# Optimization experiments

Measured on AMD Instinct MI355X. Metric: run time of the kernel, lower is better.

Reference implementation:

```python
import jax, jax.numpy as jnp
import numpy as np

B, T, D = 32, 512, 1024
EPS = 1e-12  # torch F.normalize eps


def smooth_l1(x):
    # nn.SmoothL1Loss default beta=1.0
    a = jnp.abs(x)
    return jnp.where(a < 1.0, 0.5 * x * x, a - 0.5)


def setup_inputs() -> dict:
    key = jax.random.key(0)
    k1, k2, k3, k4 = jax.random.split(key, 4)
    return {
        "word_targets": jax.random.normal(k1, (B, T, D), dtype=jnp.float32),
        "image_targets": jax.random.normal(k2, (B, D), dtype=jnp.float32),
        "preds": jax.random.normal(k3, (B, T, D), dtype=jnp.float32),
        "decode_lengths": jax.random.randint(k4, (B,), 1, T + 1, dtype=jnp.int32),
    }


def reference(word_targets, image_targets, preds, decode_lengths):
    # mask over valid (ragged) positions: [B, T]
    mask = (jnp.arange(T)[None, :] < decode_lengths[:, None]).astype(preds.dtype)
    lens = decode_lengths.astype(preds.dtype)  # [B]

    # word loss: per-sample mean of smooth_l1 over valid tokens x D
    sl1 = smooth_l1(preds - word_targets) * mask[:, :, None]  # [B,T,D]
    word_per_b = sl1.sum(axis=(1, 2)) / (lens * D)             # [B]
    word_loss = word_per_b.mean()

    # per-sentence means over valid tokens: [B, D]
    pred_mean = (preds * mask[:, :, None]).sum(axis=1) / lens[:, None]
    targ_mean = (word_targets * mask[:, :, None]).sum(axis=1) / lens[:, None]
    sentence_loss = smooth_l1(pred_mean - targ_mean).mean(axis=1).mean()

    # image embedding loss: compare pred sentence mean to L2-normalized image embedding
    norm = jnp.maximum(jnp.linalg.norm(image_targets, axis=-1, keepdims=True), EPS)
    img_norm = image_targets / norm
    image_loss = smooth_l1(pred_mean - img_norm).mean(axis=1).mean()

    return word_loss + sentence_loss + image_loss
```

## Files before the change

kernel.cpp:

```cpp
#include <hip/hip_runtime.h>
#include <math.h>

static constexpr int B_ = 32;
static constexpr int T_ = 512;
static constexpr int D_ = 1024;
static constexpr int NCH_ = 4;
static constexpr int TCH_ = T_ / NCH_;
static constexpr int NDQ_ = 4;
static constexpr float EPS_ = 1e-12f;

__device__ __forceinline__ float sl1f(float x) {
    float a = fabsf(x);
    return a < 1.0f ? 0.5f * x * x : a - 0.5f;
}

__device__ __forceinline__ float blockReduce256(float v, float* lds) {
#pragma unroll
    for (int o = 32; o > 0; o >>= 1) v += __shfl_down(v, o, 64);
    int wid = threadIdx.x >> 6, lane = threadIdx.x & 63;
    if (lane == 0) lds[wid] = v;
    __syncthreads();
    float tot = lds[0] + lds[1] + lds[2] + lds[3];
    __syncthreads();
    return tot;
}

__global__ __launch_bounds__(256, 2) void pass1_kernel(
    const float* __restrict__ preds, const float* __restrict__ wtarg,
    const int* __restrict__ lens,
    float* __restrict__ wsPred, float* __restrict__ wsTarg,
    float* __restrict__ wsSl1, float* __restrict__ out)
{
    __shared__ float4 redP[4][64];
    __shared__ float4 redT[4][64];
    __shared__ float lred[4];

    const int c = blockIdx.x, b = blockIdx.y, q = blockIdx.z;
    const int tid = threadIdx.x;
    if (c == 0 && b == 0 && q == 0 && tid == 0) out[0] = 0.f;

    const int len = lens[b];
    const int t0 = c * TCH_;
    if (t0 >= len) return;
    const int nrows = min(TCH_, len - t0);

    const int j = tid & 63;
    const int r4 = tid >> 6;

    const float4* pp = reinterpret_cast<const float4*>(preds)
                       + (size_t)(b * T_ + t0) * (D_ / 4) + q * 64 + j;
    const float4* pw = reinterpret_cast<const float4*>(wtarg)
                       + (size_t)(b * T_ + t0) * (D_ / 4) + q * 64 + j;

    float4 ps = make_float4(0.f, 0.f, 0.f, 0.f);
    float4 ts = make_float4(0.f, 0.f, 0.f, 0.f);
    float s = 0.f;

    if (nrows == TCH_) {
#pragma unroll
        for (int tt = 0; tt < 4; ++tt) {
            float4 p[8], w[8];
#pragma unroll
            for (int jj = 0; jj < 8; ++jj)
                p[jj] = pp[(size_t)(r4 + 4 * (tt * 8 + jj)) * (D_ / 4)];
#pragma unroll
            for (int jj = 0; jj < 8; ++jj)
                w[jj] = pw[(size_t)(r4 + 4 * (tt * 8 + jj)) * (D_ / 4)];
#pragma unroll
            for (int jj = 0; jj < 8; ++jj) {
                ps.x += p[jj].x; ps.y += p[jj].y; ps.z += p[jj].z; ps.w += p[jj].w;
                ts.x += w[jj].x; ts.y += w[jj].y; ts.z += w[jj].z; ts.w += w[jj].w;
                s += sl1f(p[jj].x - w[jj].x) + sl1f(p[jj].y - w[jj].y)
                   + sl1f(p[jj].z - w[jj].z) + sl1f(p[jj].w - w[jj].w);
            }
        }
    } else {
        for (int r = r4; r < nrows; r += 4) {
            float4 p = pp[(size_t)r * (D_ / 4)];
            float4 w = pw[(size_t)r * (D_ / 4)];
            ps.x += p.x; ps.y += p.y; ps.z += p.z; ps.w += p.w;
            ts.x += w.x; ts.y += w.y; ts.z += w.z; ts.w += w.w;
            s += sl1f(p.x - w.x) + sl1f(p.y - w.y) + sl1f(p.z - w.z) + sl1f(p.w - w.w);
        }
    }

    redP[r4][j] = ps;
    redT[r4][j] = ts;
    float tot = blockReduce256(s, lred);
    if (tid < 64) {
        float4 a0 = redP[0][tid], a1 = redP[1][tid], a2 = redP[2][tid], a3 = redP[3][tid];
        float4 ap = make_float4(a0.x + a1.x + a2.x + a3.x, a0.y + a1.y + a2.y + a3.y,
                                a0.z + a1.z + a2.z + a3.z, a0.w + a1.w + a2.w + a3.w);
        float4 b0 = redT[0][tid], b1 = redT[1][tid], b2 = redT[2][tid], b3 = redT[3][tid];
        float4 at = make_float4(b0.x + b1.x + b2.x + b3.x, b0.y + b1.y + b2.y + b3.y,
                                b0.z + b1.z + b2.z + b3.z, b0.w + b1.w + b2.w + b3.w);
        const size_t off = ((size_t)(b * NCH_ + c)) * (D_ / 4) + q * 64 + tid;
        reinterpret_cast<float4*>(wsPred)[off] = ap;
        reinterpret_cast<float4*>(wsTarg)[off] = at;
    }
    if (tid == 0) wsSl1[(b * NCH_ + c) * NDQ_ + q] = tot;
}

__global__ __launch_bounds__(256) void pass2_kernel(
    const float* __restrict__ img, const int* __restrict__ lens,
    const float* __restrict__ wsPred, const float* __restrict__ wsTarg,
    const float* __restrict__ wsSl1, float* __restrict__ out)
{
    __shared__ float lred[4];
    const int b = blockIdx.x, tid = threadIdx.x;
    const int len = lens[b];
    const float flen = (float)len;
    const int nc = (len + TCH_ - 1) / TCH_;

    const float4* img4 = reinterpret_cast<const float4*>(img);
    float4 im = img4[(size_t)b * (D_ / 4) + tid];
    float ss = im.x * im.x + im.y * im.y + im.z * im.z + im.w * im.w;
    float sumsq = blockReduce256(ss, lred);
    float inv_norm = 1.0f / fmaxf(sqrtf(sumsq), EPS_);

    float4 ps = make_float4(0.f, 0.f, 0.f, 0.f);
    float4 ts = make_float4(0.f, 0.f, 0.f, 0.f);
#pragma unroll
    for (int c = 0; c < NCH_; ++c) {
        if (c < nc) {
            const size_t off = ((size_t)(b * NCH_ + c)) * (D_ / 4) + tid;
            float4 p = reinterpret_cast<const float4*>(wsPred)[off];
            float4 w = reinterpret_cast<const float4*>(wsTarg)[off];
            ps.x += p.x; ps.y += p.y; ps.z += p.z; ps.w += p.w;
            ts.x += w.x; ts.y += w.y; ts.z += w.z; ts.w += w.w;
        }
    }

    const float pmx = ps.x / flen, pmy = ps.y / flen, pmz = ps.z / flen, pmw = ps.w / flen;
    const float tmx = ts.x / flen, tmy = ts.y / flen, tmz = ts.z / flen, tmw = ts.w / flen;

    float s = sl1f(pmx - tmx) + sl1f(pmy - tmy) + sl1f(pmz - tmz) + sl1f(pmw - tmw)
            + sl1f(pmx - im.x * inv_norm) + sl1f(pmy - im.y * inv_norm)
            + sl1f(pmz - im.z * inv_norm) + sl1f(pmw - im.w * inv_norm);
    float tot = blockReduce256(s, lred);

    float wv = 0.f;
    if (tid < NCH_ * NDQ_) {
        int c = tid >> 2;
        if (c < nc) wv = wsSl1[(b * NCH_ + c) * NDQ_ + (tid & 3)];
    }
    if (tid < 64) {
#pragma unroll
        for (int o = 32; o > 0; o >>= 1) wv += __shfl_down(wv, o, 64);
    }

    if (tid == 0) {
        float per_b = tot / (float)D_ + wv / (flen * (float)D_);
        atomicAdd(out, per_b * (1.0f / (float)B_));
    }
}

extern "C" void kernel_launch(void* const* d_in, const int* in_sizes, int n_in,
                              void* d_out, int out_size, void* d_ws, size_t ws_size,
                              hipStream_t stream) {
    const float* wtarg = (const float*)d_in[0];
    const float* img   = (const float*)d_in[1];
    const float* preds = (const float*)d_in[2];
    const int*   lens  = (const int*)d_in[3];
    float* out = (float*)d_out;

    float* wsPred = (float*)d_ws;
    float* wsTarg = wsPred + (size_t)B_ * NCH_ * D_;
    float* wsSl1  = wsTarg + (size_t)B_ * NCH_ * D_;

    pass1_kernel<<<dim3(NCH_, B_, NDQ_), 256, 0, stream>>>(
        preds, wtarg, lens, wsPred, wsTarg, wsSl1, out);
    pass2_kernel<<<B_, 256, 0, stream>>>(img, lens, wsPred, wsTarg, wsSl1, out);
}
```

Baseline: 28.66 us.

## Compact ragged work units with prefix scan and persistent grid-stride pass1

Replaces the fixed 4x32x4 grid, where blocks beyond a sample's length exit immediately, with a prefix-sum over per-sample valid windows that builds a compact list of work units (64-row window by 128-column slice). A fixed grid of 1024 blocks walks that list with binary search, so only valid rows are launched and the load is spread more evenly across CUs. Pass2 recomputes the same scan to gather the variable number of partials per sample. Smaller units raise occupancy but add per-unit scan, search and reduction overhead, plus more partial sums in the workspace.

```diff
diff --git a/kernel.cpp b/kernel.cpp
--- a/kernel.cpp
+++ b/kernel.cpp
@@ -4,9 +4,10 @@
 static constexpr int B_ = 32;
 static constexpr int T_ = 512;
 static constexpr int D_ = 1024;
-static constexpr int NCH_ = 4;
-static constexpr int TCH_ = T_ / NCH_;
-static constexpr int NDQ_ = 4;
+static constexpr int WROWS_ = 64;
+static constexpr int SLICE4_ = 32;
+static constexpr int NSL_ = (D_ / 4) / SLICE4_;
+static constexpr int GRID1_ = 1024;
 static constexpr float EPS_ = 1e-12f;
 
 __device__ __forceinline__ float sl1f(float x) {
@@ -25,80 +26,112 @@
     return tot;
 }
 
-__global__ __launch_bounds__(256, 2) void pass1_kernel(
+__global__ __launch_bounds__(256, 4) void pass1_kernel(
     const float* __restrict__ preds, const float* __restrict__ wtarg,
     const int* __restrict__ lens,
     float* __restrict__ wsPred, float* __restrict__ wsTarg,
     float* __restrict__ wsSl1, float* __restrict__ out)
 {
-    __shared__ float4 redP[4][64];
-    __shared__ float4 redT[4][64];
+    __shared__ float4 redP[8][SLICE4_];
+    __shared__ float4 redT[8][SLICE4_];
     __shared__ float lred[4];
-
-    const int c = blockIdx.x, b = blockIdx.y, q = blockIdx.z;
+    __shared__ int sEx[B_ + 1];
+    __shared__ int sNwin[B_];
+    __shared__ int sLen[B_];
+
     const int tid = threadIdx.x;
-    if (c == 0 && b == 0 && q == 0 && tid == 0) out[0] = 0.f;
-
-    const int len = lens[b];
-    const int t0 = c * TCH_;
-    if (t0 >= len) return;
-    const int nrows = min(TCH_, len - t0);
-
-    const int j = tid & 63;
-    const int r4 = tid >> 6;
-
-    const float4* pp = reinterpret_cast<const float4*>(preds)
-                       + (size_t)(b * T_ + t0) * (D_ / 4) + q * 64 + j;
-    const float4* pw = reinterpret_cast<const float4*>(wtarg)
-                       + (size_t)(b * T_ + t0) * (D_ / 4) + q * 64 + j;
-
-    float4 ps = make_float4(0.f, 0.f, 0.f, 0.f);
-    float4 ts = make_float4(0.f, 0.f, 0.f, 0.f);
-    float s = 0.f;
-
-    if (nrows == TCH_) {
-#pragma unroll
-        for (int tt = 0; tt < 4; ++tt) {
-            float4 p[8], w[8];
-#pragma unroll
-            for (int jj = 0; jj < 8; ++jj)
-                p[jj] = pp[(size_t)(r4 + 4 * (tt * 8 + jj)) * (D_ / 4)];
-#pragma unroll
-            for (int jj = 0; jj < 8; ++jj)
-                w[jj] = pw[(size_t)(r4 + 4 * (tt * 8 + jj)) * (D_ / 4)];
-#pragma unroll
-            for (int jj = 0; jj < 8; ++jj) {
-                ps.x += p[jj].x; ps.y += p[jj].y; ps.z += p[jj].z; ps.w += p[jj].w;
-                ts.x += w[jj].x; ts.y += w[jj].y; ts.z += w[jj].z; ts.w += w[jj].w;
-                s += sl1f(p[jj].x - w[jj].x) + sl1f(p[jj].y - w[jj].y)
-                   + sl1f(p[jj].z - w[jj].z) + sl1f(p[jj].w - w[jj].w);
+    if (blockIdx.x == 0 && tid == 0) out[0] = 0.f;
+
+    if (tid < 64) {
+        int len_t = (tid < B_) ? lens[tid] : 0;
+        int nwin = (len_t + WROWS_ - 1) / WROWS_;
+        int nu = nwin * NSL_;
+        int incl = nu;
+#pragma unroll
+        for (int o = 1; o < 64; o <<= 1) {
+            int u = __shfl_up(incl, o, 64);
+            if (tid >= o) incl += u;
+        }
+        if (tid < B_) { sEx[tid] = incl - nu; sNwin[tid] = nwin; sLen[tid] = len_t; }
+        if (tid == B_ - 1) sEx[B_] = incl;
+    }
+    __syncthreads();
+    const int total = sEx[B_];
+
+    const int j = tid & (SLICE4_ - 1);
+    const int r8 = tid >> 5;
+
+    for (int fu = blockIdx.x; fu < total; fu += GRID1_) {
+        int lo = 0, hi = B_;
+        while (hi - lo > 1) {
+            int mid = (lo + hi) >> 1;
+            if (sEx[mid] <= fu) lo = mid; else hi = mid;
+        }
+        const int b = lo;
+        const int rem = fu - sEx[b];
+        const int nwin = sNwin[b];
+        const int s = rem / nwin;
+        const int w = rem - s * nwin;
+        const int len = sLen[b];
+        const int t0 = w * WROWS_;
+        const int nr = min(WROWS_, len - t0);
+
+        const float4* pp = reinterpret_cast<const float4*>(preds)
+                           + (size_t)(b * T_ + t0) * (D_ / 4) + s * SLICE4_ + j;
+        const float4* pw = reinterpret_cast<const float4*>(wtarg)
+                           + (size_t)(b * T_ + t0) * (D_ / 4) + s * SLICE4_ + j;
+
+        float4 ps = make_float4(0.f, 0.f, 0.f, 0.f);
+        float4 ts = make_float4(0.f, 0.f, 0.f, 0.f);
+        float sl = 0.f;
+
+        if (nr == WROWS_) {
+            float4 p[8], wv[8];
+#pragma unroll
+            for (int k = 0; k < 8; ++k) p[k] = pp[(size_t)(r8 + 8 * k) * (D_ / 4)];
+#pragma unroll
+            for (int k = 0; k < 8; ++k) wv[k] = pw[(size_t)(r8 + 8 * k) * (D_ / 4)];
+#pragma unroll
+            for (int k = 0; k < 8; ++k) {
+                ps.x += p[k].x; ps.y += p[k].y; ps.z += p[k].z; ps.w += p[k].w;
+                ts.x += wv[k].x; ts.y += wv[k].y; ts.z += wv[k].z; ts.w += wv[k].w;
+                sl += sl1f(p[k].x - wv[k].x) + sl1f(p[k].y - wv[k].y)
+                    + sl1f(p[k].z - wv[k].z) + sl1f(p[k].w - wv[k].w);
             }
-        }
-    } else {
-        for (int r = r4; r < nrows; r += 4) {
-            float4 p = pp[(size_t)r * (D_ / 4)];
-            float4 w = pw[(size_t)r * (D_ / 4)];
-            ps.x += p.x; ps.y += p.y; ps.z += p.z; ps.w += p.w;
-            ts.x += w.x; ts.y += w.y; ts.z += w.z; ts.w += w.w;
-            s += sl1f(p.x - w.x) + sl1f(p.y - w.y) + sl1f(p.z - w.z) + sl1f(p.w - w.w);
-        }
-    }
-
-    redP[r4][j] = ps;
-    redT[r4][j] = ts;
-    float tot = blockReduce256(s, lred);
-    if (tid < 64) {
-        float4 a0 = redP[0][tid], a1 = redP[1][tid], a2 = redP[2][tid], a3 = redP[3][tid];
-        float4 ap = make_float4(a0.x + a1.x + a2.x + a3.x, a0.y + a1.y + a2.y + a3.y,
-                                a0.z + a1.z + a2.z + a3.z, a0.w + a1.w + a2.w + a3.w);
-        float4 b0 = redT[0][tid], b1 = redT[1][tid], b2 = redT[2][tid], b3 = redT[3][tid];
-        float4 at = make_float4(b0.x + b1.x + b2.x + b3.x, b0.y + b1.y + b2.y + b3.y,
-                                b0.z + b1.z + b2.z + b3.z, b0.w + b1.w + b2.w + b3.w);
-        const size_t off = ((size_t)(b * NCH_ + c)) * (D_ / 4) + q * 64 + tid;
-        reinterpret_cast<float4*>(wsPred)[off] = ap;
-        reinterpret_cast<float4*>(wsTarg)[off] = at;
-    }
-    if (tid == 0) wsSl1[(b * NCH_ + c) * NDQ_ + q] = tot;
+        } else {
+            for (int k = 0; k < 8; ++k) {
+                int r = r8 + 8 * k;
+                if (r < nr) {
+                    float4 p = pp[(size_t)r * (D_ / 4)];
+                    float4 wv = pw[(size_t)r * (D_ / 4)];
+                    ps.x += p.x; ps.y += p.y; ps.z += p.z; ps.w += p.w;
+                    ts.x += wv.x; ts.y += wv.y; ts.z += wv.z; ts.w += wv.w;
+                    sl += sl1f(p.x - wv.x) + sl1f(p.y - wv.y)
+                        + sl1f(p.z - wv.z) + sl1f(p.w - wv.w);
+                }
+            }
+        }
+
+        redP[r8][j] = ps;
+        redT[r8][j] = ts;
+        float tot = blockReduce256(sl, lred);
+
+        if (tid < SLICE4_) {
+            float4 ap = make_float4(0.f, 0.f, 0.f, 0.f);
+            float4 at = make_float4(0.f, 0.f, 0.f, 0.f);
+#pragma unroll
+            for (int k = 0; k < 8; ++k) {
+                float4 a = redP[k][tid], bb = redT[k][tid];
+                ap.x += a.x; ap.y += a.y; ap.z += a.z; ap.w += a.w;
+                at.x += bb.x; at.y += bb.y; at.z += bb.z; at.w += bb.w;
+            }
+            const size_t off = (size_t)fu * SLICE4_ + tid;
+            reinterpret_cast<float4*>(wsPred)[off] = ap;
+            reinterpret_cast<float4*>(wsTarg)[off] = at;
+        }
+        if (tid == 0) wsSl1[fu] = tot;
+        __syncthreads();
+    }
 }
 
 __global__ __launch_bounds__(256) void pass2_kernel(
@@ -107,10 +140,40 @@
     const float* __restrict__ wsSl1, float* __restrict__ out)
 {
     __shared__ float lred[4];
+    __shared__ int sEx[B_ + 1];
+    __shared__ int sNwin[B_];
+
     const int b = blockIdx.x, tid = threadIdx.x;
+    if (tid < 64) {
+        int len_t = (tid < B_) ? lens[tid] : 0;
+        int nwin = (len_t + WROWS_ - 1) / WROWS_;
+        int nu = nwin * NSL_;
+        int incl = nu;
+#pragma unroll
+        for (int o = 1; o < 64; o <<= 1) {
+            int u = __shfl_up(incl, o, 64);
+            if (tid >= o) incl += u;
+        }
+        if (tid < B_) { sEx[tid] = incl - nu; sNwin[tid] = nwin; }
+        if (tid == B_ - 1) sEx[B_] = incl;
+    }
+    __syncthreads();
+
+    const int base = sEx[b];
+    const int nwin = sNwin[b];
     const int len = lens[b];
     const float flen = (float)len;
-    const int nc = (len + TCH_ - 1) / TCH_;
+    const int s = tid >> 5, col = tid & 31;
+
+    float4 ps = make_float4(0.f, 0.f, 0.f, 0.f);
+    float4 ts = make_float4(0.f, 0.f, 0.f, 0.f);
+    for (int w = 0; w < nwin; ++w) {
+        const size_t off = (size_t)(base + s * nwin + w) * SLICE4_ + col;
+        float4 p = reinterpret_cast<const float4*>(wsPred)[off];
+        float4 t = reinterpret_cast<const float4*>(wsTarg)[off];
+        ps.x += p.x; ps.y += p.y; ps.z += p.z; ps.w += p.w;
+        ts.x += t.x; ts.y += t.y; ts.z += t.z; ts.w += t.w;
+    }
 
     const float4* img4 = reinterpret_cast<const float4*>(img);
     float4 im = img4[(size_t)b * (D_ / 4) + tid];
@@ -118,32 +181,15 @@
     float sumsq = blockReduce256(ss, lred);
     float inv_norm = 1.0f / fmaxf(sqrtf(sumsq), EPS_);
 
-    float4 ps = make_float4(0.f, 0.f, 0.f, 0.f);
-    float4 ts = make_float4(0.f, 0.f, 0.f, 0.f);
-#pragma unroll
-    for (int c = 0; c < NCH_; ++c) {
-        if (c < nc) {
-            const size_t off = ((size_t)(b * NCH_ + c)) * (D_ / 4) + tid;
-            float4 p = reinterpret_cast<const float4*>(wsPred)[off];
-            float4 w = reinterpret_cast<const float4*>(wsTarg)[off];
-            ps.x += p.x; ps.y += p.y; ps.z += p.z; ps.w += p.w;
-            ts.x += w.x; ts.y += w.y; ts.z += w.z; ts.w += w.w;
-        }
-    }
-
     const float pmx = ps.x / flen, pmy = ps.y / flen, pmz = ps.z / flen, pmw = ps.w / flen;
     const float tmx = ts.x / flen, tmy = ts.y / flen, tmz = ts.z / flen, tmw = ts.w / flen;
 
-    float s = sl1f(pmx - tmx) + sl1f(pmy - tmy) + sl1f(pmz - tmz) + sl1f(pmw - tmw)
-            + sl1f(pmx - im.x * inv_norm) + sl1f(pmy - im.y * inv_norm)
-            + sl1f(pmz - im.z * inv_norm) + sl1f(pmw - im.w * inv_norm);
-    float tot = blockReduce256(s, lred);
-
-    float wv = 0.f;
-    if (tid < NCH_ * NDQ_) {
-        int c = tid >> 2;
-        if (c < nc) wv = wsSl1[(b * NCH_ + c) * NDQ_ + (tid & 3)];
-    }
+    float sv = sl1f(pmx - tmx) + sl1f(pmy - tmy) + sl1f(pmz - tmz) + sl1f(pmw - tmw)
+             + sl1f(pmx - im.x * inv_norm) + sl1f(pmy - im.y * inv_norm)
+             + sl1f(pmz - im.z * inv_norm) + sl1f(pmw - im.w * inv_norm);
+    float tot = blockReduce256(sv, lred);
+
+    float wv = (tid < nwin * NSL_) ? wsSl1[base + tid] : 0.f;
     if (tid < 64) {
 #pragma unroll
         for (int o = 32; o > 0; o >>= 1) wv += __shfl_down(wv, o, 64);
@@ -165,10 +211,10 @@
     float* out = (float*)d_out;
 
     float* wsPred = (float*)d_ws;
-    float* wsTarg = wsPred + (size_t)B_ * NCH_ * D_;
-    float* wsSl1  = wsTarg + (size_t)B_ * NCH_ * D_;
-
-    pass1_kernel<<<dim3(NCH_, B_, NDQ_), 256, 0, stream>>>(
-        preds, wtarg, lens, wsPred, wsTarg, wsSl1, out);
+    float* wsTarg = wsPred + (size_t)2048 * 128;
+    float* wsSl1  = wsTarg + (size_t)2048 * 128;
+
+    pass1_kernel<<<GRID1_, 256, 0, stream>>>(preds, wtarg, lens,
+                                             wsPred, wsTarg, wsSl1, out);
     pass2_kernel<<<B_, 256, 0, stream>>>(img, lens, wsPred, wsTarg, wsSl1, out);
 }
```

New measurement: 25.91 us. -9.6%, faster.
